# Performance work log

Measured on AMD Instinct MI355X. Metric: run time of the kernel, lower is better.

## Reference

```python
import jax, jax.numpy as jnp
import numpy as np

DIM = 2048
STATE = 16
BATCH = 2
SEQ = 2048
LN_EPS = 1e-5


def setup_inputs() -> dict:
    key = jax.random.key(0)
    ks = jax.random.split(key, 12)
    d, n = DIM, STATE
    inp = {
        "x": jax.random.normal(ks[0], (BATCH, SEQ, d), dtype=jnp.float32),
        "ln_gamma": jnp.ones((d,), dtype=jnp.float32),
        "ln_beta": jnp.zeros((d,), dtype=jnp.float32),
        # proj_in: Linear(d, 2d) (spectral-normed; weights treated as effective)
        "W_in": jax.random.normal(ks[1], (2 * d, d), dtype=jnp.float32) / np.sqrt(d),
        "b_in": jnp.zeros((2 * d,), dtype=jnp.float32),
        "state_A": jax.random.normal(ks[2], (n, d), dtype=jnp.float32) * 0.01,
        "W_B": jax.random.normal(ks[3], (n, d), dtype=jnp.float32) / np.sqrt(d),
        "b_B": jnp.zeros((n,), dtype=jnp.float32),
        "W_C": jax.random.normal(ks[4], (n, d), dtype=jnp.float32) / np.sqrt(d),
        "b_C": jnp.zeros((n,), dtype=jnp.float32),
        "W_dt": jax.random.normal(ks[5], (d, d), dtype=jnp.float32) / np.sqrt(d),
        "b_dt": jnp.zeros((d,), dtype=jnp.float32),
        "W_out": jax.random.normal(ks[6], (d, d), dtype=jnp.float32) / np.sqrt(d),
        "b_out": jnp.zeros((d,), dtype=jnp.float32),
    }
    return inp


def reference(x, ln_gamma, ln_beta, W_in, b_in, state_A, W_B, b_B, W_C, b_C,
              W_dt, b_dt, W_out, b_out):
    residual = x
    # LayerNorm over last dim
    mu = jnp.mean(x, axis=-1, keepdims=True)
    var = jnp.mean(jnp.square(x - mu), axis=-1, keepdims=True)
    xn = (x - mu) * jax.lax.rsqrt(var + LN_EPS) * ln_gamma + ln_beta
    # input projection and gate split
    xz = jnp.einsum('bsd,ed->bse', xn, W_in) + b_in          # (B,S,2D)
    x_ssm, z = jnp.split(xz, 2, axis=-1)                      # (B,S,D) each
    # dt = clamp(softplus(proj_dt(x_ssm)), max=1.0)
    dt = jnp.minimum(jax.nn.softplus(jnp.einsum('bsd,ed->bse', x_ssm, W_dt) + b_dt), 1.0)
    Bm = jnp.einsum('bsd,nd->bsn', x_ssm, W_B) + b_B          # (B,S,N)
    Cm = jnp.einsum('bsd,nd->bsn', x_ssm, W_C) + b_C          # (B,S,N)
    # A_bar[b,s,n,d] = exp(state_A[n,d] * dt[b,s,d])
    A_bar = jnp.exp(state_A[None, None, :, :] * dt[:, :, None, :])  # (B,S,N,D)
    # y[b,s,d] = sum_n C[b,s,n]*B[b,s,n]*A_bar[b,s,n,d] * x_ssm[b,s,d]
    y = jnp.einsum('bsn,bsnd->bsd', Cm * Bm, A_bar) * x_ssm
    gated = y * jax.nn.silu(z)
    out = jnp.einsum('bsd,ed->bse', gated, W_out) + b_out
    return out + residual
```

## Files before the change

kernel.cpp:

```cpp
#include <hip/hip_runtime.h>

typedef unsigned short u16;
typedef float f32x4 __attribute__((ext_vector_type(4)));
typedef __bf16 bf16x8 __attribute__((ext_vector_type(8)));

__device__ __forceinline__ u16 f2bf(float f) {
    unsigned u = __float_as_uint(f);
    u += 0x7FFFu + ((u >> 16) & 1u);
    return (u16)(u >> 16);
}
__device__ __forceinline__ float b2f(u16 h) {
    return __uint_as_float(((unsigned)h) << 16);
}

__device__ __forceinline__ void async16(const u16* g, u16* l) {
    __builtin_amdgcn_global_load_lds(
        (__attribute__((address_space(1))) void*)(u16*)g,
        (__attribute__((address_space(3))) void*)l,
        16, 0, 0);
}

#define T_TOK 4096
#define DIM   2048

__global__ __launch_bounds__(256) void castln_kernel(const float* __restrict__ W_in,
                                                     u16* __restrict__ wb_in,
                                                     const float* __restrict__ x,
                                                     const float* __restrict__ g,
                                                     const float* __restrict__ b,
                                                     u16* __restrict__ o) {
    __shared__ float s1[4], s2[4];
    int blk = blockIdx.x, tid = threadIdx.x;
    if (blk < 8192) {
        int i = blk * 256 + tid;
        float4 f = ((const float4*)W_in)[i];
        ushort4 u;
        u.x = f2bf(f.x); u.y = f2bf(f.y); u.z = f2bf(f.z); u.w = f2bf(f.w);
        ((ushort4*)wb_in)[i] = u;
        return;
    }
    int t = blk - 8192;
    int wave = tid >> 6, lane = tid & 63;
    size_t base = (size_t)t * DIM;
    int d0 = tid * 8;
    float4 v0 = *(const float4*)(x + base + d0);
    float4 v1 = *(const float4*)(x + base + d0 + 4);
    float v[8] = {v0.x, v0.y, v0.z, v0.w, v1.x, v1.y, v1.z, v1.w};
    float s = 0.f;
#pragma unroll
    for (int j = 0; j < 8; ++j) s += v[j];
#pragma unroll
    for (int o2 = 32; o2; o2 >>= 1) s += __shfl_xor(s, o2);
    if (lane == 0) s1[wave] = s;
    __syncthreads();
    float mu = (s1[0] + s1[1] + s1[2] + s1[3]) * (1.f / DIM);
    float q = 0.f;
#pragma unroll
    for (int j = 0; j < 8; ++j) { float dd = v[j] - mu; q += dd * dd; }
#pragma unroll
    for (int o2 = 32; o2; o2 >>= 1) q += __shfl_xor(q, o2);
    if (lane == 0) s2[wave] = q;
    __syncthreads();
    float var = (s2[0] + s2[1] + s2[2] + s2[3]) * (1.f / DIM);
    float rs = rsqrtf(var + 1e-5f);
    float4 g0 = *(const float4*)(g + d0), g1 = *(const float4*)(g + d0 + 4);
    float4 b0 = *(const float4*)(b + d0), b1 = *(const float4*)(b + d0 + 4);
    float gv[8] = {g0.x, g0.y, g0.z, g0.w, g1.x, g1.y, g1.z, g1.w};
    float bv[8] = {b0.x, b0.y, b0.z, b0.w, b1.x, b1.y, b1.z, b1.w};
    ushort4 r0, r1;
    u16* rp0 = (u16*)&r0; u16* rp1 = (u16*)&r1;
#pragma unroll
    for (int j = 0; j < 4; ++j) {
        rp0[j] = f2bf((v[j] - mu) * rs * gv[j] + bv[j]);
        rp1[j] = f2bf((v[j + 4] - mu) * rs * gv[j + 4] + bv[j + 4]);
    }
    *(ushort4*)(o + base + d0) = r0;
    *(ushort4*)(o + base + d0 + 4) = r1;
}

__global__ __launch_bounds__(256) void cast4_kernel(const float* __restrict__ s0, u16* __restrict__ d0, int n0,
                                                    const float* __restrict__ s1, u16* __restrict__ d1, int n1,
                                                    const float* __restrict__ s2, u16* __restrict__ d2, int n2,
                                                    const float* __restrict__ s3, u16* __restrict__ d3, int n3) {
    int j = blockIdx.x * 256 + threadIdx.x;
    const float* s; u16* d;
    if (j < n0) { s = s0; d = d0; }
    else {
        j -= n0;
        if (j < n1) { s = s1; d = d1; }
        else {
            j -= n1;
            if (j < n2) { s = s2; d = d2; }
            else { j -= n2; if (j >= n3) return; s = s3; d = d3; }
        }
    }
    float4 f = ((const float4*)s)[j];
    ushort4 u;
    u.x = f2bf(f.x); u.y = f2bf(f.y); u.z = f2bf(f.z); u.w = f2bf(f.w);
    ((ushort4*)d)[j] = u;
}

#define GBM 256
#define GBN 256
#define GBK 64

#define WAITV2 asm volatile("s_waitcnt vmcnt(2)" ::: "memory")

__global__ __launch_bounds__(512) void gemm_wide(const u16* __restrict__ A,
                                                 const u16* __restrict__ W,
                                                 const float* __restrict__ bias,
                                                 u16* __restrict__ Xs,
                                                 u16* __restrict__ Z, int K) {
    __shared__ __align__(16) u16 lA[2][GBM * GBK];
    __shared__ __align__(16) u16 lB[2][GBN * GBK];
    const int tid = threadIdx.x;
    const int wv = tid >> 6, lane = tid & 63;
    const int quad = lane >> 4, l16 = lane & 15;
    const int wr = wv >> 2, wc = wv & 3;
    const int tM = blockIdx.x * GBM, tN = blockIdx.y * GBN;

    const int srow = tid >> 3;
    const int swz = ((tid & 7) ^ (srow & 7)) * 8;
    const u16* gA = A + (size_t)(tM + srow) * 2048 + swz;
    const u16* gW = W + (size_t)(tN + srow) * 2048 + swz;

#define STAGE_AH(BI, KC, H) do {                                              \
    _Pragma("unroll") for (int r_ = 2 * (H); r_ < 2 * (H) + 2; ++r_)          \
      async16(gA + (size_t)r_ * 64 * 2048 + (KC),                             \
              &lA[BI][(r_ * 64 + wv * 8) * GBK]);                             \
  } while (0)
#define STAGE_BH(BI, KC, H) do {                                              \
    _Pragma("unroll") for (int r_ = 2 * (H); r_ < 2 * (H) + 2; ++r_)          \
      async16(gW + (size_t)r_ * 64 * 2048 + (KC),                             \
              &lB[BI][(r_ * 64 + wv * 8) * GBK]);                             \
  } while (0)

    int aoff[2][4][2], boff[2][2][2];
#pragma unroll
    for (int qm = 0; qm < 2; ++qm)
#pragma unroll
        for (int mi = 0; mi < 4; ++mi)
#pragma unroll
            for (int h = 0; h < 2; ++h) {
                int row = wr * 128 + (qm * 4 + mi) * 16 + l16;
                aoff[qm][mi][h] = row * GBK + (((h * 4 + quad) ^ (l16 & 7)) * 8);
            }
#pragma unroll
    for (int qn = 0; qn < 2; ++qn)
#pragma unroll
        for (int ni = 0; ni < 2; ++ni)
#pragma unroll
            for (int h = 0; h < 2; ++h) {
                int row = wc * 64 + (qn * 2 + ni) * 16 + l16;
                boff[qn][ni][h] = row * GBK + (((h * 4 + quad) ^ (l16 & 7)) * 8);
            }

    f32x4 acc[8][4] = {};
    bf16x8 af[4][2];

#define PHASE(BI, QM, QN, LOADA, STAGE_STMT, WAIT_STMT) do {                  \
    if (LOADA) {                                                              \
      _Pragma("unroll") for (int mi_ = 0; mi_ < 4; ++mi_)                     \
        _Pragma("unroll") for (int h_ = 0; h_ < 2; ++h_)                      \
          af[mi_][h_] = *(const bf16x8*)&lA[BI][aoff[QM][mi_][h_]];           \
    }                                                                         \
    bf16x8 bfr_[2][2];                                                        \
    _Pragma("unroll") for (int ni_ = 0; ni_ < 2; ++ni_)                       \
      _Pragma("unroll") for (int h_ = 0; h_ < 2; ++h_)                        \
        bfr_[ni_][h_] = *(const bf16x8*)&lB[BI][boff[QN][ni_][h_]];           \
    STAGE_STMT;                                                               \
    __builtin_amdgcn_s_setprio(1);                                            \
    _Pragma("unroll") for (int mi_ = 0; mi_ < 4; ++mi_)                       \
      _Pragma("unroll") for (int ni_ = 0; ni_ < 2; ++ni_)                     \
        _Pragma("unroll") for (int h_ = 0; h_ < 2; ++h_)                      \
          acc[QM * 4 + mi_][QN * 2 + ni_] =                                   \
              __builtin_amdgcn_mfma_f32_16x16x32_bf16(                        \
                  af[mi_][h_], bfr_[ni_][h_],                                 \
                  acc[QM * 4 + mi_][QN * 2 + ni_], 0, 0, 0);                  \
    __builtin_amdgcn_s_setprio(0);                                            \
    WAIT_STMT;                                                                \
    __builtin_amdgcn_s_barrier();                                             \
  } while (0)

    STAGE_AH(0, 0, 0);
    STAGE_AH(0, 0, 1);
    STAGE_BH(0, 0, 0);
    STAGE_BH(0, 0, 1);
    STAGE_AH(1, 64, 0);
    WAITV2;
    __builtin_amdgcn_s_barrier();

    const int NIT = K >> 7;
    for (int it = 0; it < NIT; ++it) {
        const int k1 = it * 128 + 64;
        int kn = it * 128 + 128;
        if (kn > K - 64) kn = K - 64;
        int kn1 = it * 128 + 192;
        if (kn1 > K - 64) kn1 = K - 64;

        PHASE(0, 0, 0, 1, STAGE_AH(1, k1, 1),  (void)0);
        PHASE(0, 0, 1, 0, STAGE_BH(1, k1, 0),  (void)0);
        PHASE(0, 1, 0, 1, STAGE_BH(1, k1, 1),  (void)0);
        PHASE(0, 1, 1, 0, STAGE_AH(0, kn, 0),  WAITV2);
        PHASE(1, 0, 0, 1, STAGE_AH(0, kn, 1),  (void)0);
        PHASE(1, 0, 1, 0, STAGE_BH(0, kn, 0),  (void)0);
        PHASE(1, 1, 0, 1, STAGE_BH(0, kn, 1),  (void)0);
        PHASE(1, 1, 1, 0, STAGE_AH(1, kn1, 0), WAITV2);
    }

    asm volatile("s_waitcnt vmcnt(0)" ::: "memory");

    const bool isb_z = (tN >= 2048);
    u16* dst = isb_z ? Z : Xs;
#pragma unroll
    for (int mi = 0; mi < 8; ++mi) {
#pragma unroll
        for (int ni = 0; ni < 4; ++ni) {
            int col = tN + wc * 64 + ni * 16 + l16;
            float bv = bias[col];
            int ocol = isb_z ? (col - 2048) : col;
#pragma unroll
            for (int r = 0; r < 4; ++r) {
                int row = tM + wr * 128 + mi * 16 + quad * 4 + r;
                dst[(size_t)row * 2048 + ocol] = f2bf(acc[mi][ni][r] + bv);
            }
        }
    }
#undef PHASE
#undef STAGE_AH
#undef STAGE_BH
}

#define NBM 128
#define NBN 64
#define NBK 64

template <int EPI>
__global__ __launch_bounds__(256) void gemm_nw(const u16* __restrict__ A, int lda,
                                               const u16* __restrict__ W, int ldw,
                                               const float* __restrict__ bias,
                                               const float* __restrict__ resid,
                                               void* __restrict__ C, int ldc, int K,
                                               u16* __restrict__ dots) {
    __shared__ __align__(16) u16 lAB[(NBM + NBN) * NBK];
    const int tid = threadIdx.x;
    const int wave = tid >> 6, lane = tid & 63;
    const int quad = lane >> 4, l16 = lane & 15;
    const int tM = blockIdx.x * NBM;
    const int tN = blockIdx.y * NBN;
    const int wr = wave >> 1, wc = wave & 1;

    const int rowin = tid >> 3;
    const int r3 = rowin & 7;
    const int col8 = ((tid & 7) ^ r3) * 8;
    const u16* gptr[6];
    u16* ldst[6];
#pragma unroll
    for (int i = 0; i < 6; ++i) {
        int trow = i * 32 + rowin;
        const u16* src = (i < 4) ? (A + (size_t)(tM + trow) * lda)
                                 : (W + (size_t)(tN + (trow - NBM)) * ldw);
        gptr[i] = src + col8;
        ldst[i] = &lAB[(i * 32 + wave * 8) * NBK];
    }

    int a_off[2][4], b_off[2][2];
#pragma unroll
    for (int h = 0; h < 2; ++h) {
#pragma unroll
        for (int mi = 0; mi < 4; ++mi)
            a_off[h][mi] = (wr * 64 + mi * 16 + l16) * NBK +
                           (((h * 4 + quad) ^ (l16 & 7)) * 8);
#pragma unroll
        for (int ni = 0; ni < 2; ++ni)
            b_off[h][ni] = (NBM + wc * 32 + ni * 16 + l16) * NBK +
                           (((h * 4 + quad) ^ (l16 & 7)) * 8);
    }

    f32x4 acc[4][2] = {};

    for (int kt = 0; kt < K; kt += NBK) {
#pragma unroll
        for (int i = 0; i < 6; ++i) async16(gptr[i] + kt, ldst[i]);
        __syncthreads();
        bf16x8 af[2][4], bfr[2][2];
#pragma unroll
        for (int h = 0; h < 2; ++h) {
#pragma unroll
            for (int mi = 0; mi < 4; ++mi) af[h][mi] = *(const bf16x8*)&lAB[a_off[h][mi]];
#pragma unroll
            for (int ni = 0; ni < 2; ++ni) bfr[h][ni] = *(const bf16x8*)&lAB[b_off[h][ni]];
        }
#pragma unroll
        for (int h = 0; h < 2; ++h)
#pragma unroll
            for (int mi = 0; mi < 4; ++mi)
#pragma unroll
                for (int ni = 0; ni < 2; ++ni)
                    acc[mi][ni] = __builtin_amdgcn_mfma_f32_16x16x32_bf16(
                        af[h][mi], bfr[h][ni], acc[mi][ni], 0, 0, 0);
        __syncthreads();
    }

#pragma unroll
    for (int mi = 0; mi < 4; ++mi) {
#pragma unroll
        for (int ni = 0; ni < 2; ++ni) {
            int col = tN + wc * 32 + ni * 16 + l16;
            float bv = (EPI == 1 && col >= 2048) ? 0.f : bias[col];
#pragma unroll
            for (int r = 0; r < 4; ++r) {
                int row = tM + wr * 64 + mi * 16 + quad * 4 + r;
                float v = acc[mi][ni][r] + bv;
                if constexpr (EPI == 1) {
                    if (col < 2048) {
                        float sp = (v > 0.5413f) ? 1.0f
                                                 : __logf(1.0f + __expf(v));
                        ((u16*)C)[(size_t)row * ldc + col] = f2bf(sp);
                    } else if (col < 2080) {
                        dots[(size_t)row * 32 + (col - 2048)] = f2bf(v);
                    }
                } else {
                    size_t idx = (size_t)row * ldc + col;
                    ((float*)C)[idx] = v + resid[idx];
                }
            }
        }
    }
}

__global__ __launch_bounds__(256) void ssm_gate2_kernel(const u16* __restrict__ dtb,
                                                        const u16* __restrict__ xsb,
                                                        const u16* __restrict__ zb,
                                                        const float* __restrict__ A,
                                                        const u16* __restrict__ dots,
                                                        const float* __restrict__ bB,
                                                        const float* __restrict__ bC,
                                                        u16* __restrict__ gated) {
    __shared__ float Pl[8][16];
    const int tid = threadIdx.x;
    const int t0 = blockIdx.x * 8;
    const int d0 = tid * 8;

    float a[16][8];
#pragma unroll
    for (int n = 0; n < 16; ++n) {
        float4 a0 = *(const float4*)(A + n * DIM + d0);
        float4 a1 = *(const float4*)(A + n * DIM + d0 + 4);
        a[n][0] = a0.x; a[n][1] = a0.y; a[n][2] = a0.z; a[n][3] = a0.w;
        a[n][4] = a1.x; a[n][5] = a1.y; a[n][6] = a1.z; a[n][7] = a1.w;
    }
    if (tid < 128) {
        int tt = tid >> 4, n = tid & 15;
        float Bv = b2f(dots[(size_t)(t0 + tt) * 32 + n]) + bB[n];
        float Cv = b2f(dots[(size_t)(t0 + tt) * 32 + 16 + n]) + bC[n];
        Pl[tt][n] = Bv * Cv;
    }
    __syncthreads();

    for (int tt = 0; tt < 8; ++tt) {
        size_t dbase = (size_t)(t0 + tt) * DIM;
        ushort4 dth0 = *(const ushort4*)(dtb + dbase + d0);
        ushort4 dth1 = *(const ushort4*)(dtb + dbase + d0 + 4);
        ushort4 xsh0 = *(const ushort4*)(xsb + dbase + d0);
        ushort4 xsh1 = *(const ushort4*)(xsb + dbase + d0 + 4);
        ushort4 zh0  = *(const ushort4*)(zb + dbase + d0);
        ushort4 zh1  = *(const ushort4*)(zb + dbase + d0 + 4);
        float dtv[8], xsv[8], zv[8];
        const u16* dp0 = (const u16*)&dth0; const u16* dp1 = (const u16*)&dth1;
        const u16* xp0 = (const u16*)&xsh0; const u16* xp1 = (const u16*)&xsh1;
        const u16* zp0 = (const u16*)&zh0;  const u16* zp1 = (const u16*)&zh1;
#pragma unroll
        for (int j = 0; j < 4; ++j) {
            dtv[j] = b2f(dp0[j]); dtv[j + 4] = b2f(dp1[j]);
            xsv[j] = b2f(xp0[j]); xsv[j + 4] = b2f(xp1[j]);
            zv[j]  = b2f(zp0[j]); zv[j + 4]  = b2f(zp1[j]);
        }
        float s[8] = {};
#pragma unroll
        for (int n = 0; n < 16; ++n) {
            float pn = Pl[tt][n];
#pragma unroll
            for (int j = 0; j < 8; ++j) s[j] += pn * __expf(a[n][j] * dtv[j]);
        }
        ushort4 r0, r1;
        u16* rp0 = (u16*)&r0; u16* rp1 = (u16*)&r1;
#pragma unroll
        for (int j = 0; j < 8; ++j) {
            float y = s[j] * xsv[j];
            float sz = zv[j] * (1.0f / (1.0f + __expf(-zv[j])));
            u16 hv = f2bf(y * sz);
            if (j < 4) rp0[j] = hv; else rp1[j - 4] = hv;
        }
        *(ushort4*)(gated + dbase + d0) = r0;
        *(ushort4*)(gated + dbase + d0 + 4) = r1;
    }
}

extern "C" void kernel_launch(void* const* d_in, const int* in_sizes, int n_in,
                              void* d_out, int out_size, void* d_ws, size_t ws_size,
                              hipStream_t stream) {
    const float* x      = (const float*)d_in[0];
    const float* ln_g   = (const float*)d_in[1];
    const float* ln_b   = (const float*)d_in[2];
    const float* W_in   = (const float*)d_in[3];
    const float* b_in   = (const float*)d_in[4];
    const float* stateA = (const float*)d_in[5];
    const float* W_B    = (const float*)d_in[6];
    const float* b_B    = (const float*)d_in[7];
    const float* W_C    = (const float*)d_in[8];
    const float* b_C    = (const float*)d_in[9];
    const float* W_dt   = (const float*)d_in[10];
    const float* b_dt   = (const float*)d_in[11];
    const float* W_out  = (const float*)d_in[12];
    const float* b_out  = (const float*)d_in[13];

    char* ws = (char*)d_ws;
    u16*   wb_in  = (u16*)(ws);
    u16*   wb_out = (u16*)(ws);
    u16*   xnb    = (u16*)(ws + 16777216);
    u16*   wb_dt  = (u16*)(ws + 16777216);
    u16*   gated  = (u16*)(ws + 16777216);
    u16*   xsb    = (u16*)(ws + 33554432);
    u16*   zb     = (u16*)(ws + 50331648);
    u16*   dtb    = (u16*)(ws + 67108864);
    u16*   dotsb  = (u16*)(ws + 83886080);

    castln_kernel<<<12288, 256, 0, stream>>>(W_in, wb_in, x, ln_g, ln_b, xnb);
    gemm_wide<<<dim3(16, 16), 512, 0, stream>>>(xnb, wb_in, b_in, xsb, zb, 2048);
    cast4_kernel<<<8256, 256, 0, stream>>>(
        W_dt, wb_dt, 1048576,
        W_B,  wb_dt + (size_t)2048 * 2048, 8192,
        W_C,  wb_dt + (size_t)2064 * 2048, 8192,
        W_out, wb_out, 1048576);
    gemm_nw<1><<<dim3(32, 33), 256, 0, stream>>>(xsb, 2048, wb_dt, 2048, b_dt,
                                                 nullptr, dtb, 2048, 2048, dotsb);
    ssm_gate2_kernel<<<512, 256, 0, stream>>>(dtb, xsb, zb, stateA, dotsb,
                                              b_B, b_C, gated);
    gemm_nw<2><<<dim3(32, 32), 256, 0, stream>>>(gated, 2048, wb_out, 2048, b_out,
                                                 x, (float*)d_out, 2048, 2048, nullptr);
}
```

Before: 355.4 us.

## Merge weight casts into LN kernel and enlarge narrow GEMM tiles to 128x128

```diff
diff --git a/kernel.cpp b/kernel.cpp
--- a/kernel.cpp
+++ b/kernel.cpp
@@ -23,23 +23,36 @@
 #define T_TOK 4096
 #define DIM   2048
 
-__global__ __launch_bounds__(256) void castln_kernel(const float* __restrict__ W_in,
-                                                     u16* __restrict__ wb_in,
-                                                     const float* __restrict__ x,
-                                                     const float* __restrict__ g,
-                                                     const float* __restrict__ b,
-                                                     u16* __restrict__ o) {
+__global__ __launch_bounds__(256) void castln_all(const float* __restrict__ W_in,
+                                                  u16* __restrict__ wb_in,
+                                                  const float* __restrict__ W_dt,
+                                                  u16* __restrict__ wb_dt,
+                                                  const float* __restrict__ W_B,
+                                                  const float* __restrict__ W_C,
+                                                  const float* __restrict__ W_out,
+                                                  u16* __restrict__ wb_out,
+                                                  const float* __restrict__ x,
+                                                  const float* __restrict__ g,
+                                                  const float* __restrict__ b,
+                                                  u16* __restrict__ o) {
     __shared__ float s1[4], s2[4];
     int blk = blockIdx.x, tid = threadIdx.x;
-    if (blk < 8192) {
-        int i = blk * 256 + tid;
-        float4 f = ((const float4*)W_in)[i];
+    if (blk < 16448) {
+        const float* s; u16* d; int j;
+        if (blk < 8192)       { s = W_in;  d = wb_in;  j = blk * 256 + tid; }
+        else if (blk < 12288) { s = W_dt;  d = wb_dt;  j = (blk - 8192) * 256 + tid; }
+        else if (blk < 12320) { s = W_B;   d = wb_dt + (size_t)2048 * 2048;
+                                j = (blk - 12288) * 256 + tid; }
+        else if (blk < 12352) { s = W_C;   d = wb_dt + (size_t)2064 * 2048;
+                                j = (blk - 12320) * 256 + tid; }
+        else                  { s = W_out; d = wb_out; j = (blk - 12352) * 256 + tid; }
+        float4 f = ((const float4*)s)[j];
         ushort4 u;
         u.x = f2bf(f.x); u.y = f2bf(f.y); u.z = f2bf(f.z); u.w = f2bf(f.w);
-        ((ushort4*)wb_in)[i] = u;
+        ((ushort4*)d)[j] = u;
         return;
     }
-    int t = blk - 8192;
+    int t = blk - 16448;
     int wave = tid >> 6, lane = tid & 63;
     size_t base = (size_t)t * DIM;
     int d0 = tid * 8;
@@ -76,28 +89,6 @@
     }
     *(ushort4*)(o + base + d0) = r0;
     *(ushort4*)(o + base + d0 + 4) = r1;
-}
-
-__global__ __launch_bounds__(256) void cast4_kernel(const float* __restrict__ s0, u16* __restrict__ d0, int n0,
-                                                    const float* __restrict__ s1, u16* __restrict__ d1, int n1,
-                                                    const float* __restrict__ s2, u16* __restrict__ d2, int n2,
-                                                    const float* __restrict__ s3, u16* __restrict__ d3, int n3) {
-    int j = blockIdx.x * 256 + threadIdx.x;
-    const float* s; u16* d;
-    if (j < n0) { s = s0; d = d0; }
-    else {
-        j -= n0;
-        if (j < n1) { s = s1; d = d1; }
-        else {
-            j -= n1;
-            if (j < n2) { s = s2; d = d2; }
-            else { j -= n2; if (j >= n3) return; s = s3; d = d3; }
-        }
-    }
-    float4 f = ((const float4*)s)[j];
-    ushort4 u;
-    u.x = f2bf(f.x); u.y = f2bf(f.y); u.z = f2bf(f.z); u.w = f2bf(f.w);
-    ((ushort4*)d)[j] = u;
 }
 
 #define GBM 256
@@ -231,98 +222,95 @@
 #undef STAGE_BH
 }
 
-#define NBM 128
-#define NBN 64
-#define NBK 64
+#define DBM 128
+#define DBN 128
+#define DBK 64
 
 template <int EPI>
-__global__ __launch_bounds__(256) void gemm_nw(const u16* __restrict__ A, int lda,
-                                               const u16* __restrict__ W, int ldw,
+__global__ __launch_bounds__(256) void gemm128(const u16* __restrict__ A,
+                                               const u16* __restrict__ W,
                                                const float* __restrict__ bias,
                                                const float* __restrict__ resid,
-                                               void* __restrict__ C, int ldc, int K,
-                                               u16* __restrict__ dots) {
-    __shared__ __align__(16) u16 lAB[(NBM + NBN) * NBK];
+                                               void* __restrict__ C,
+                                               u16* __restrict__ dots, int K) {
+    __shared__ __align__(16) u16 lAB[(DBM + DBN) * DBK];
     const int tid = threadIdx.x;
     const int wave = tid >> 6, lane = tid & 63;
     const int quad = lane >> 4, l16 = lane & 15;
-    const int tM = blockIdx.x * NBM;
-    const int tN = blockIdx.y * NBN;
+    const int tM = blockIdx.x * DBM;
+    const int tN = blockIdx.y * DBN;
     const int wr = wave >> 1, wc = wave & 1;
 
     const int rowin = tid >> 3;
-    const int r3 = rowin & 7;
-    const int col8 = ((tid & 7) ^ r3) * 8;
-    const u16* gptr[6];
-    u16* ldst[6];
-#pragma unroll
-    for (int i = 0; i < 6; ++i) {
+    const int col8 = ((tid & 7) ^ (rowin & 7)) * 8;
+    const u16* gptr[8];
+    u16* ldst[8];
+#pragma unroll
+    for (int i = 0; i < 8; ++i) {
         int trow = i * 32 + rowin;
-        const u16* src = (i < 4) ? (A + (size_t)(tM + trow) * lda)
-                                 : (W + (size_t)(tN + (trow - NBM)) * ldw);
+        const u16* src = (i < 4) ? (A + (size_t)(tM + trow) * 2048)
+                                 : (W + (size_t)(tN + (trow - DBM)) * 2048);
         gptr[i] = src + col8;
-        ldst[i] = &lAB[(i * 32 + wave * 8) * NBK];
-    }
-
-    int a_off[2][4], b_off[2][2];
+        ldst[i] = &lAB[(i * 32 + wave * 8) * DBK];
+    }
+
+    int a_off[2][4], b_off[2][4];
 #pragma unroll
     for (int h = 0; h < 2; ++h) {
 #pragma unroll
         for (int mi = 0; mi < 4; ++mi)
-            a_off[h][mi] = (wr * 64 + mi * 16 + l16) * NBK +
+            a_off[h][mi] = (wr * 64 + mi * 16 + l16) * DBK +
                            (((h * 4 + quad) ^ (l16 & 7)) * 8);
 #pragma unroll
-        for (int ni = 0; ni < 2; ++ni)
-            b_off[h][ni] = (NBM + wc * 32 + ni * 16 + l16) * NBK +
+        for (int ni = 0; ni < 4; ++ni)
+            b_off[h][ni] = (DBM + wc * 64 + ni * 16 + l16) * DBK +
                            (((h * 4 + quad) ^ (l16 & 7)) * 8);
     }
 
-    f32x4 acc[4][2] = {};
-
-    for (int kt = 0; kt < K; kt += NBK) {
-#pragma unroll
-        for (int i = 0; i < 6; ++i) async16(gptr[i] + kt, ldst[i]);
+    f32x4 acc[4][4] = {};
+
+    for (int kt = 0; kt < K; kt += DBK) {
+#pragma unroll
+        for (int i = 0; i < 8; ++i) async16(gptr[i] + kt, ldst[i]);
         __syncthreads();
-        bf16x8 af[2][4], bfr[2][2];
 #pragma unroll
         for (int h = 0; h < 2; ++h) {
-#pragma unroll
-            for (int mi = 0; mi < 4; ++mi) af[h][mi] = *(const bf16x8*)&lAB[a_off[h][mi]];
-#pragma unroll
-            for (int ni = 0; ni < 2; ++ni) bfr[h][ni] = *(const bf16x8*)&lAB[b_off[h][ni]];
-        }
-#pragma unroll
-        for (int h = 0; h < 2; ++h)
+            bf16x8 af[4], bfr[4];
+#pragma unroll
+            for (int i = 0; i < 4; ++i) af[i] = *(const bf16x8*)&lAB[a_off[h][i]];
+#pragma unroll
+            for (int i = 0; i < 4; ++i) bfr[i] = *(const bf16x8*)&lAB[b_off[h][i]];
 #pragma unroll
             for (int mi = 0; mi < 4; ++mi)
 #pragma unroll
-                for (int ni = 0; ni < 2; ++ni)
+                for (int ni = 0; ni < 4; ++ni)
                     acc[mi][ni] = __builtin_amdgcn_mfma_f32_16x16x32_bf16(
-                        af[h][mi], bfr[h][ni], acc[mi][ni], 0, 0, 0);
+                        af[mi], bfr[ni], acc[mi][ni], 0, 0, 0);
+        }
         __syncthreads();
     }
 
 #pragma unroll
     for (int mi = 0; mi < 4; ++mi) {
 #pragma unroll
-        for (int ni = 0; ni < 2; ++ni) {
-            int col = tN + wc * 32 + ni * 16 + l16;
-            float bv = (EPI == 1 && col >= 2048) ? 0.f : bias[col];
+        for (int ni = 0; ni < 4; ++ni) {
+            int col = tN + wc * 64 + ni * 16 + l16;
 #pragma unroll
             for (int r = 0; r < 4; ++r) {
                 int row = tM + wr * 64 + mi * 16 + quad * 4 + r;
-                float v = acc[mi][ni][r] + bv;
                 if constexpr (EPI == 1) {
                     if (col < 2048) {
+                        float v = acc[mi][ni][r] + bias[col];
                         float sp = (v > 0.5413f) ? 1.0f
                                                  : __logf(1.0f + __expf(v));
-                        ((u16*)C)[(size_t)row * ldc + col] = f2bf(sp);
+                        ((u16*)C)[(size_t)row * 2048 + col] = f2bf(sp);
                     } else if (col < 2080) {
-                        dots[(size_t)row * 32 + (col - 2048)] = f2bf(v);
+                        dots[(size_t)row * 32 + (col - 2048)] =
+                            f2bf(acc[mi][ni][r]);
                     }
                 } else {
-                    size_t idx = (size_t)row * ldc + col;
-                    ((float*)C)[idx] = v + resid[idx];
+                    size_t idx = (size_t)row * 2048 + col;
+                    ((float*)C)[idx] = acc[mi][ni][r] + bias[col] + resid[idx];
                 }
             }
         }
@@ -331,12 +319,11 @@
 
 __global__ __launch_bounds__(256) void ssm_gate2_kernel(const u16* __restrict__ dtb,
                                                         const u16* __restrict__ xsb,
-                                                        const u16* __restrict__ zb,
+                                                        u16* __restrict__ zg,
                                                         const float* __restrict__ A,
                                                         const u16* __restrict__ dots,
                                                         const float* __restrict__ bB,
-                                                        const float* __restrict__ bC,
-                                                        u16* __restrict__ gated) {
+                                                        const float* __restrict__ bC) {
     __shared__ float Pl[8][16];
     const int tid = threadIdx.x;
     const int t0 = blockIdx.x * 8;
@@ -364,8 +351,8 @@
         ushort4 dth1 = *(const ushort4*)(dtb + dbase + d0 + 4);
         ushort4 xsh0 = *(const ushort4*)(xsb + dbase + d0);
         ushort4 xsh1 = *(const ushort4*)(xsb + dbase + d0 + 4);
-        ushort4 zh0  = *(const ushort4*)(zb + dbase + d0);
-        ushort4 zh1  = *(const ushort4*)(zb + dbase + d0 + 4);
+        ushort4 zh0  = *(const ushort4*)(zg + dbase + d0);
+        ushort4 zh1  = *(const ushort4*)(zg + dbase + d0 + 4);
         float dtv[8], xsv[8], zv[8];
         const u16* dp0 = (const u16*)&dth0; const u16* dp1 = (const u16*)&dth1;
         const u16* xp0 = (const u16*)&xsh0; const u16* xp1 = (const u16*)&xsh1;
@@ -392,8 +379,8 @@
             u16 hv = f2bf(y * sz);
             if (j < 4) rp0[j] = hv; else rp1[j - 4] = hv;
         }
-        *(ushort4*)(gated + dbase + d0) = r0;
-        *(ushort4*)(gated + dbase + d0 + 4) = r1;
+        *(ushort4*)(zg + dbase + d0) = r0;
+        *(ushort4*)(zg + dbase + d0 + 4) = r1;
     }
 }
 
@@ -417,26 +404,21 @@
 
     char* ws = (char*)d_ws;
     u16*   wb_in  = (u16*)(ws);
-    u16*   wb_out = (u16*)(ws);
+    u16*   dotsb  = (u16*)(ws);
     u16*   xnb    = (u16*)(ws + 16777216);
-    u16*   wb_dt  = (u16*)(ws + 16777216);
-    u16*   gated  = (u16*)(ws + 16777216);
+    u16*   dtb    = (u16*)(ws + 16777216);
     u16*   xsb    = (u16*)(ws + 33554432);
-    u16*   zb     = (u16*)(ws + 50331648);
-    u16*   dtb    = (u16*)(ws + 67108864);
-    u16*   dotsb  = (u16*)(ws + 83886080);
-
-    castln_kernel<<<12288, 256, 0, stream>>>(W_in, wb_in, x, ln_g, ln_b, xnb);
-    gemm_wide<<<dim3(16, 16), 512, 0, stream>>>(xnb, wb_in, b_in, xsb, zb, 2048);
-    cast4_kernel<<<8256, 256, 0, stream>>>(
-        W_dt, wb_dt, 1048576,
-        W_B,  wb_dt + (size_t)2048 * 2048, 8192,
-        W_C,  wb_dt + (size_t)2064 * 2048, 8192,
-        W_out, wb_out, 1048576);
-    gemm_nw<1><<<dim3(32, 33), 256, 0, stream>>>(xsb, 2048, wb_dt, 2048, b_dt,
-                                                 nullptr, dtb, 2048, 2048, dotsb);
-    ssm_gate2_kernel<<<512, 256, 0, stream>>>(dtb, xsb, zb, stateA, dotsb,
-                                              b_B, b_C, gated);
-    gemm_nw<2><<<dim3(32, 32), 256, 0, stream>>>(gated, 2048, wb_out, 2048, b_out,
-                                                 x, (float*)d_out, 2048, 2048, nullptr);
-}
+    u16*   zg     = (u16*)(ws + 50331648);
+    u16*   wb_dt  = (u16*)(ws + 67108864);
+    u16*   wb_out = (u16*)(ws + 75759616);
+
+    castln_all<<<20544, 256, 0, stream>>>(W_in, wb_in, W_dt, wb_dt, W_B, W_C,
+                                          W_out, wb_out, x, ln_g, ln_b, xnb);
+    gemm_wide<<<dim3(16, 16), 512, 0, stream>>>(xnb, wb_in, b_in, xsb, zg, 2048);
+    gemm128<1><<<dim3(32, 17), 256, 0, stream>>>(xsb, wb_dt, b_dt, nullptr,
+                                                 dtb, dotsb, 2048);
+    ssm_gate2_kernel<<<512, 256, 0, stream>>>(dtb, xsb, zg, stateA, dotsb,
+                                              b_B, b_C);
+    gemm128<2><<<dim3(32, 16), 256, 0, stream>>>(zg, wb_out, b_out, x,
+                                                 (float*)d_out, nullptr, 2048);
+}
```

Result: slower. 396.0 us (+11.4%).
